# Kernel optimization log

Hardware: AMD Instinct MI355X
Metric: run time of the kernel (lower is better)

Reference implementation:

```python
import jax, jax.numpy as jnp
import numpy as np

B, T, D, H = 4, 2048, 1024, 16
HD = D // H  # head_dim = 64


def setup_inputs() -> dict:
    key = jax.random.key(0)
    ks = jax.random.split(key, 9)
    s = 1.0 / np.sqrt(D)
    return {
        "x": jax.random.normal(ks[0], (B, T, D), dtype=jnp.float32),
        "Wq": jax.random.normal(ks[1], (D, D), dtype=jnp.float32) * s,
        "bq": jax.random.normal(ks[2], (D,), dtype=jnp.float32) * 0.01,
        "Wk": jax.random.normal(ks[3], (D, D), dtype=jnp.float32) * s,
        "bk": jax.random.normal(ks[4], (D,), dtype=jnp.float32) * 0.01,
        "Wv": jax.random.normal(ks[5], (D, D), dtype=jnp.float32) * s,
        "bv": jax.random.normal(ks[6], (D,), dtype=jnp.float32) * 0.01,
        "Wp": jax.random.normal(ks[7], (D, D), dtype=jnp.float32) * s,
        "bp": jax.random.normal(ks[8], (D,), dtype=jnp.float32) * 0.01,
    }


def reference(x, Wq, bq, Wk, bk, Wv, bv, Wp, bp):
    # Linear projections (weights stored as [in, out]; torch Linear is x @ W.T + b,
    # here we store the already-transposed matrix so math is identical)
    q = (x @ Wq + bq).reshape(B, T, H, HD).transpose(0, 2, 1, 3)  # [B,H,T,HD]
    k = (x @ Wk + bk).reshape(B, T, H, HD).transpose(0, 2, 1, 3)
    v = (x @ Wv + bv).reshape(B, T, H, HD).transpose(0, 2, 1, 3)

    scores = jnp.einsum("bhqd,bhkd->bhqk", q, k) / jnp.sqrt(jnp.float32(HD))
    causal = jnp.tril(jnp.ones((T, T), dtype=bool))  # keep lower triangle
    scores = jnp.where(causal, scores, -jnp.inf)
    attn = jax.nn.softmax(scores, axis=-1)  # dropout is identity at eval
    out = jnp.einsum("bhqk,bhkd->bhqd", attn, v)  # [B,H,T,HD]
    out = out.transpose(0, 2, 1, 3).reshape(B, T, D)
    return out @ Wp + bp
```

## Files before the change

kernel.cpp:

```cpp
#include <hip/hip_runtime.h>
#include <hip/hip_bf16.h>

#define BB 4
#define TT 2048
#define DD 1024
#define HH 16
#define HD 64
#define MM (BB*TT)

typedef __attribute__((ext_vector_type(8))) _Float16 f16x8;
typedef __attribute__((ext_vector_type(4))) float f32x4;

static __device__ __forceinline__ void gload_lds16(const void* g, void* l) {
  __builtin_amdgcn_global_load_lds((const __attribute__((address_space(1))) void*)g,
                                   (__attribute__((address_space(3))) void*)l, 16, 0, 0);
}

__global__ __launch_bounds__(256) void cvt_f16(const float* __restrict__ in,
                                               _Float16* __restrict__ out, int n8) {
  int i = blockIdx.x * 256 + threadIdx.x;
  if (i >= n8) return;
  const f32x4* p = (const f32x4*)in;
  f32x4 a = p[2*i];
  f32x4 b = p[2*i+1];
  f16x8 r;
  r[0]=(_Float16)a[0]; r[1]=(_Float16)a[1]; r[2]=(_Float16)a[2]; r[3]=(_Float16)a[3];
  r[4]=(_Float16)b[0]; r[5]=(_Float16)b[1]; r[6]=(_Float16)b[2]; r[7]=(_Float16)b[3];
  *(f16x8*)(out + (size_t)8*i) = r;
}

__global__ __launch_bounds__(256) void transpose_cvt(
    const float* __restrict__ W0, const float* __restrict__ W1,
    const float* __restrict__ W2, const float* __restrict__ W3,
    _Float16* __restrict__ O0, _Float16* __restrict__ O1,
    _Float16* __restrict__ O2, _Float16* __restrict__ O3) {
  const float* W; _Float16* O;
  switch (blockIdx.z) {
    case 0: W = W0; O = O0; break;
    case 1: W = W1; O = O1; break;
    case 2: W = W2; O = O2; break;
    default: W = W3; O = O3; break;
  }
  __shared__ float tile[32][33];
  int bx = blockIdx.x * 32, by = blockIdx.y * 32;
  int tx = threadIdx.x, ty = threadIdx.y;
#pragma unroll
  for (int i = 0; i < 4; i++)
    tile[ty + 8*i][tx] = W[(size_t)(by + ty + 8*i) * DD + bx + tx];
  __syncthreads();
#pragma unroll
  for (int i = 0; i < 4; i++)
    O[(size_t)(bx + ty + 8*i) * DD + by + tx] = (_Float16)tile[tx][ty + 8*i];
}

template<bool OUT_F32>
static __device__ __forceinline__ void gemm_body(
    const _Float16* __restrict__ A, const _Float16* __restrict__ Bt,
    const float* __restrict__ bias, void* __restrict__ Cv) {
  const int K = 1024, N = 1024;
  __shared__ __align__(16) _Float16 Alds[128*32];
  __shared__ __align__(16) _Float16 Blds[128*32];
  int tid = threadIdx.x;
  int wid = tid >> 6, lane = tid & 63;
  int m0 = blockIdx.y * 128, n0 = blockIdx.x * 128;
  int wr = wid >> 1, wc = wid & 1;
  int lr = lane & 15, lk = lane >> 4;

  f32x4 zf = {0.f, 0.f, 0.f, 0.f};
  f32x4 acc[4][4];
#pragma unroll
  for (int m = 0; m < 4; m++)
#pragma unroll
    for (int n = 0; n < 4; n++) acc[m][n] = zf;

  int c0 = wid * 2;
  int srow = c0 * 16 + (lane >> 2);
  int skc  = (lane & 3) * 8;
  const _Float16* gA0 = A  + (size_t)(m0 + srow) * K + skc;
  const _Float16* gA1 = gA0 + 16 * K;
  const _Float16* gB0 = Bt + (size_t)(n0 + srow) * K + skc;
  const _Float16* gB1 = gB0 + 16 * K;
  _Float16* lA0 = Alds + c0 * 512;
  _Float16* lA1 = Alds + (c0 + 1) * 512;
  _Float16* lB0 = Blds + c0 * 512;
  _Float16* lB1 = Blds + (c0 + 1) * 512;

  for (int k0 = 0; k0 < K; k0 += 32) {
    __syncthreads();
    gload_lds16(gA0 + k0, lA0);
    gload_lds16(gA1 + k0, lA1);
    gload_lds16(gB0 + k0, lB0);
    gload_lds16(gB1 + k0, lB1);
    __syncthreads();
    f16x8 af[4], bf[4];
#pragma unroll
    for (int m = 0; m < 4; m++)
      af[m] = *(const f16x8*)&Alds[(wr*64 + m*16 + lr)*32 + lk*8];
#pragma unroll
    for (int n = 0; n < 4; n++)
      bf[n] = *(const f16x8*)&Blds[(wc*64 + n*16 + lr)*32 + lk*8];
#pragma unroll
    for (int m = 0; m < 4; m++)
#pragma unroll
      for (int n = 0; n < 4; n++)
        acc[m][n] = __builtin_amdgcn_mfma_f32_16x16x32_f16(af[m], bf[n], acc[m][n], 0, 0, 0);
  }

#pragma unroll
  for (int n = 0; n < 4; n++) {
    int col = n0 + wc*64 + n*16 + lr;
    float bs = bias[col];
#pragma unroll
    for (int m = 0; m < 4; m++) {
      int row = m0 + wr*64 + m*16 + lk*4;
#pragma unroll
      for (int r = 0; r < 4; r++) {
        float v = acc[m][n][r] + bs;
        if (OUT_F32) ((float*)Cv)[(size_t)(row + r) * N + col] = v;
        else         ((_Float16*)Cv)[(size_t)(row + r) * N + col] = (_Float16)v;
      }
    }
  }
}

__global__ __launch_bounds__(256) void gemm_qkv(
    const _Float16* __restrict__ X,
    const _Float16* __restrict__ WqT, const _Float16* __restrict__ WkT,
    const _Float16* __restrict__ WvT,
    const float* __restrict__ bq, const float* __restrict__ bk,
    const float* __restrict__ bv,
    _Float16* __restrict__ Qo, _Float16* __restrict__ Ko, _Float16* __restrict__ Vo) {
  const _Float16* Bt; const float* bias; _Float16* C;
  if (blockIdx.z == 0)      { Bt = WqT; bias = bq; C = Qo; }
  else if (blockIdx.z == 1) { Bt = WkT; bias = bk; C = Ko; }
  else                      { Bt = WvT; bias = bv; C = Vo; }
  gemm_body<false>(X, Bt, bias, C);
}

__global__ __launch_bounds__(256) void gemm_proj(
    const _Float16* __restrict__ Ain, const _Float16* __restrict__ WpT,
    const float* __restrict__ bp, float* __restrict__ out) {
  gemm_body<true>(Ain, WpT, bp, out);
}

__global__ __launch_bounds__(256, 2) void attn_fwd(
    const _Float16* __restrict__ Q, const _Float16* __restrict__ Kg,
    const _Float16* __restrict__ Vg, _Float16* __restrict__ O) {
  __shared__ __align__(16) _Float16 Klds[2*4096];
  __shared__ __align__(16) _Float16 Vt[2*4608];
  __shared__ __align__(16) _Float16 Plds[4*32*72];

  const int tid = threadIdx.x;
  const int wid = tid >> 6, lane = tid & 63;
  const int lr = lane & 15, lk = lane >> 4;
  const int bh = blockIdx.y, b = bh >> 4, h = bh & 15;
  const size_t base = (size_t)b * TT * DD + h * HD;
  const float sc = 0.18033688011112042f;

  const int krow  = 16*wid + (lane >> 3);
  const int kchnk = ((lane & 7) ^ (lane >> 3)) * 8;
  const int kg0 = krow*DD + kchnk, kg1 = (krow+8)*DD + kchnk;
  const int kl0 = 16*wid*64,       kl1 = (16*wid+8)*64;
  const int vch = lane & 7;
  const int vg0 = krow*DD + vch*8, vg1 = (krow+8)*DD + vch*8;

  _Float16* Pw = Plds + wid*32*72;

  for (int qs = 0; qs < 2; ++qs) {
    const int qt = qs ? (15 - (int)blockIdx.x) : (int)blockIdx.x;
    const int jmax = 2*qt + 1;

    f16x8 qf[2][2];
#pragma unroll
    for (int t = 0; t < 2; ++t) {
      const size_t qr = base + (size_t)(qt*128 + wid*32 + t*16 + lr) * DD;
#pragma unroll
      for (int hh2 = 0; hh2 < 2; ++hh2)
        qf[t][hh2] = *(const f16x8*)&Q[qr + hh2*32 + lk*8];
    }

    f32x4 zf = {0.f, 0.f, 0.f, 0.f};
    f32x4 o[2][4];
    float m[2][4], l[2][4];
#pragma unroll
    for (int t = 0; t < 2; ++t)
#pragma unroll
      for (int f = 0; f < 4; ++f) o[t][f] = zf;
#pragma unroll
    for (int t = 0; t < 2; ++t)
#pragma unroll
      for (int r = 0; r < 4; ++r) { m[t][r] = -1e30f; l[t][r] = 0.f; }

    {
      gload_lds16(Kg + base + kg0, Klds + kl0);
      gload_lds16(Kg + base + kg1, Klds + kl1);
      f16x8 v0 = *(const f16x8*)(Vg + base + vg0);
      f16x8 v1 = *(const f16x8*)(Vg + base + vg1);
#pragma unroll
      for (int u = 0; u < 8; ++u) {
        int d = vch*8 + u;
        int jx0 = (krow & 7)     | ((((krow>>3)     ^ (d>>3)) & 7) << 3);
        int jx1 = ((krow+8) & 7) | (((((krow+8)>>3) ^ (d>>3)) & 7) << 3);
        Vt[d*72 + jx0] = v0[u];
        Vt[d*72 + jx1] = v1[u];
      }
      __syncthreads();
    }

    int bsel = 0;
    for (int jt = 0; jt <= jmax; ++jt) {
      const bool pf = (jt < jmax);
      f16x8 vr0, vr1;
      if (pf) {
        const size_t nb = base + (size_t)(jt+1) * 64 * DD;
        _Float16* kd = Klds + (bsel^1)*4096;
        gload_lds16(Kg + nb + kg0, kd + kl0);
        gload_lds16(Kg + nb + kg1, kd + kl1);
        vr0 = *(const f16x8*)(Vg + nb + vg0);
        vr1 = *(const f16x8*)(Vg + nb + vg1);
      }

      const _Float16* Kb = Klds + bsel*4096;
      f32x4 s[2][4];
      __builtin_amdgcn_s_setprio(1);
#pragma unroll
      for (int f = 0; f < 4; ++f) {
        const int row = 16*f + lr;
        f16x8 kf0 = *(const f16x8*)&Kb[row*64 + ((lk    ) ^ (lr & 7))*8];
        f16x8 kf1 = *(const f16x8*)&Kb[row*64 + ((lk + 4) ^ (lr & 7))*8];
#pragma unroll
        for (int t = 0; t < 2; ++t) {
          f32x4 z = zf;
          z = __builtin_amdgcn_mfma_f32_16x16x32_f16(qf[t][0], kf0, z, 0, 0, 0);
          z = __builtin_amdgcn_mfma_f32_16x16x32_f16(qf[t][1], kf1, z, 0, 0, 0);
          s[t][f] = z;
        }
      }
      __builtin_amdgcn_s_setprio(0);

#pragma unroll
      for (int t = 0; t < 2; ++t) {
        const int qmin = qt*128 + wid*32 + t*16;
        if (64*jt + 64 > qmin) {
#pragma unroll
          for (int f = 0; f < 4; ++f)
#pragma unroll
            for (int r = 0; r < 4; ++r) {
              int jg = 64*jt + 16*f + lr;
              int qg = qmin + lk*4 + r;
              s[t][f][r] = (jg <= qg) ? s[t][f][r] * sc : -1e30f;
            }
        } else {
#pragma unroll
          for (int f = 0; f < 4; ++f)
#pragma unroll
            for (int r = 0; r < 4; ++r) s[t][f][r] *= sc;
        }
        float alpha[4];
#pragma unroll
        for (int r = 0; r < 4; ++r) {
          float v = fmaxf(fmaxf(s[t][0][r], s[t][1][r]), fmaxf(s[t][2][r], s[t][3][r]));
          v = fmaxf(v, __shfl_xor(v, 1));
          v = fmaxf(v, __shfl_xor(v, 2));
          v = fmaxf(v, __shfl_xor(v, 4));
          v = fmaxf(v, __shfl_xor(v, 8));
          float mn = fmaxf(m[t][r], v);
          alpha[r] = exp2f(m[t][r] - mn);
          m[t][r] = mn;
        }
#pragma unroll
        for (int r = 0; r < 4; ++r) {
          float sum = 0.f;
#pragma unroll
          for (int f = 0; f < 4; ++f) {
            float p = exp2f(s[t][f][r] - m[t][r]);
            s[t][f][r] = p;
            sum += p;
          }
          sum += __shfl_xor(sum, 1);
          sum += __shfl_xor(sum, 2);
          sum += __shfl_xor(sum, 4);
          sum += __shfl_xor(sum, 8);
          l[t][r] = l[t][r] * alpha[r] + sum;
#pragma unroll
          for (int f = 0; f < 4; ++f) o[t][f][r] *= alpha[r];
        }
#pragma unroll
        for (int f = 0; f < 4; ++f)
#pragma unroll
          for (int r = 0; r < 4; ++r)
            Pw[(t*16 + lk*4 + r)*72 + f*16 + lr] = (_Float16)s[t][f][r];
      }

      f16x8 pa[2][2];
#pragma unroll
      for (int t = 0; t < 2; ++t)
#pragma unroll
        for (int hh2 = 0; hh2 < 2; ++hh2)
          pa[t][hh2] = *(const f16x8*)&Pw[(t*16 + lr)*72 + hh2*32 + lk*8];

      const _Float16* Vb = Vt + bsel*4608;
      __builtin_amdgcn_s_setprio(1);
#pragma unroll
      for (int f = 0; f < 4; ++f) {
        int d0 = f*16 + lr;
        int cx = (d0 >> 3) & 7;
        f16x8 vf0 = *(const f16x8*)&Vb[d0*72 + (((0*4 + lk) ^ cx) << 3)];
        f16x8 vf1 = *(const f16x8*)&Vb[d0*72 + (((1*4 + lk) ^ cx) << 3)];
#pragma unroll
        for (int t = 0; t < 2; ++t) {
          o[t][f] = __builtin_amdgcn_mfma_f32_16x16x32_f16(pa[t][0], vf0, o[t][f], 0, 0, 0);
          o[t][f] = __builtin_amdgcn_mfma_f32_16x16x32_f16(pa[t][1], vf1, o[t][f], 0, 0, 0);
        }
      }
      __builtin_amdgcn_s_setprio(0);

      if (pf) {
        _Float16* vd = Vt + (bsel^1)*4608;
#pragma unroll
        for (int u = 0; u < 8; ++u) {
          int d = vch*8 + u;
          int jx0 = (krow & 7)     | ((((krow>>3)     ^ (d>>3)) & 7) << 3);
          int jx1 = ((krow+8) & 7) | (((((krow+8)>>3) ^ (d>>3)) & 7) << 3);
          vd[d*72 + jx0] = vr0[u];
          vd[d*72 + jx1] = vr1[u];
        }
      }
      __syncthreads();
      bsel ^= 1;
    }

#pragma unroll
    for (int t = 0; t < 2; ++t) {
      float inv[4];
#pragma unroll
      for (int r = 0; r < 4; ++r) inv[r] = 1.f / l[t][r];
#pragma unroll
      for (int f = 0; f < 4; ++f) {
        int d = 16*f + lr;
#pragma unroll
        for (int r = 0; r < 4; ++r) {
          int qg = qt*128 + wid*32 + t*16 + lk*4 + r;
          O[base + (size_t)qg * DD + d] = (_Float16)(o[t][f][r] * inv[r]);
        }
      }
    }
    __syncthreads();
  }
}

extern "C" void kernel_launch(void* const* d_in, const int* in_sizes, int n_in,
                              void* d_out, int out_size, void* d_ws, size_t ws_size,
                              hipStream_t stream) {
  const float* x  = (const float*)d_in[0];
  const float* Wq = (const float*)d_in[1];
  const float* bq = (const float*)d_in[2];
  const float* Wk = (const float*)d_in[3];
  const float* bk = (const float*)d_in[4];
  const float* Wv = (const float*)d_in[5];
  const float* bv = (const float*)d_in[6];
  const float* Wp = (const float*)d_in[7];
  const float* bp = (const float*)d_in[8];
  float* out = (float*)d_out;

  const size_t XN = (size_t)MM * DD;
  const size_t WN = (size_t)DD * DD;
  _Float16* ws  = (_Float16*)d_ws;
  _Float16* Xb  = ws;
  _Float16* WqT = ws + XN;
  _Float16* WkT = WqT + WN;
  _Float16* WvT = WkT + WN;
  _Float16* WpT = WvT + WN;
  _Float16* Qb  = WpT + WN;
  _Float16* Kb  = Qb + XN;
  _Float16* Vb  = Kb + XN;
  _Float16* Ab  = Xb;

  cvt_f16<<<dim3((unsigned)(XN/8/256)), 256, 0, stream>>>(x, Xb, (int)(XN/8));
  transpose_cvt<<<dim3(32, 32, 4), dim3(32, 8), 0, stream>>>(Wq, Wk, Wv, Wp,
                                                             WqT, WkT, WvT, WpT);
  gemm_qkv<<<dim3(8, 64, 3), 256, 0, stream>>>(Xb, WqT, WkT, WvT, bq, bk, bv,
                                               Qb, Kb, Vb);
  attn_fwd<<<dim3(8, 64), 256, 0, stream>>>(Qb, Kb, Vb, Ab);
  gemm_proj<<<dim3(8, 64), 256, 0, stream>>>(Ab, WpT, bp, out);
}
```

Baseline: 335.2 us.

## Emit transposed V and prescaled Q from QKV GEMM; simplify attention loads

The QKV GEMM epilogue now writes V transposed per (batch, head) and folds the softmax scale into Q. This lets the attention kernel load V with async global-to-LDS copies instead of a register transpose, and drop the per-score multiply. Attention also stops pairing light and heavy query tiles, launching one block per tile with a higher occupancy hint, and skips the online-softmax rescale unless the running max grows by more than a threshold. The cost is uneven causal work across blocks, strided 4-element stores in the V epilogue, and less exact max tracking, which is still correct but risks precision loss.

```diff
diff --git a/kernel.cpp b/kernel.cpp
--- a/kernel.cpp
+++ b/kernel.cpp
@@ -9,7 +9,10 @@
 #define MM (BB*TT)
 
 typedef __attribute__((ext_vector_type(8))) _Float16 f16x8;
+typedef __attribute__((ext_vector_type(4))) _Float16 f16x4;
 typedef __attribute__((ext_vector_type(4))) float f32x4;
+
+#define QSCALE 0.18033688011112042f
 
 static __device__ __forceinline__ void gload_lds16(const void* g, void* l) {
   __builtin_amdgcn_global_load_lds((const __attribute__((address_space(1))) void*)g,
@@ -53,10 +56,9 @@
     O[(size_t)(bx + ty + 8*i) * DD + by + tx] = (_Float16)tile[tx][ty + 8*i];
 }
 
-template<bool OUT_F32>
 static __device__ __forceinline__ void gemm_body(
     const _Float16* __restrict__ A, const _Float16* __restrict__ Bt,
-    const float* __restrict__ bias, void* __restrict__ Cv) {
+    const float* __restrict__ bias, void* __restrict__ Cv, int mode) {
   const int K = 1024, N = 1024;
   __shared__ __align__(16) _Float16 Alds[128*32];
   __shared__ __align__(16) _Float16 Blds[128*32];
@@ -112,12 +114,27 @@
     float bs = bias[col];
 #pragma unroll
     for (int m = 0; m < 4; m++) {
-      int row = m0 + wr*64 + m*16 + lk*4;
-#pragma unroll
-      for (int r = 0; r < 4; r++) {
-        float v = acc[m][n][r] + bs;
-        if (OUT_F32) ((float*)Cv)[(size_t)(row + r) * N + col] = v;
-        else         ((_Float16*)Cv)[(size_t)(row + r) * N + col] = (_Float16)v;
+      int rowg = m0 + wr*64 + m*16 + lk*4;
+      if (mode == 2) {
+        int b = rowg >> 11, t = rowg & 2047;
+        size_t idx = ((size_t)(b*1024 + col) << 11) + t;
+        f16x4 pk;
+#pragma unroll
+        for (int r = 0; r < 4; r++) pk[r] = (_Float16)(acc[m][n][r] + bs);
+        *(f16x4*)&((_Float16*)Cv)[idx] = pk;
+      } else if (mode == 3) {
+#pragma unroll
+        for (int r = 0; r < 4; r++)
+          ((float*)Cv)[(size_t)(rowg + r) * N + col] = acc[m][n][r] + bs;
+      } else if (mode == 1) {
+#pragma unroll
+        for (int r = 0; r < 4; r++)
+          ((_Float16*)Cv)[(size_t)(rowg + r) * N + col] =
+              (_Float16)((acc[m][n][r] + bs) * QSCALE);
+      } else {
+#pragma unroll
+        for (int r = 0; r < 4; r++)
+          ((_Float16*)Cv)[(size_t)(rowg + r) * N + col] = (_Float16)(acc[m][n][r] + bs);
       }
     }
   }
@@ -129,223 +146,208 @@
     const _Float16* __restrict__ WvT,
     const float* __restrict__ bq, const float* __restrict__ bk,
     const float* __restrict__ bv,
-    _Float16* __restrict__ Qo, _Float16* __restrict__ Ko, _Float16* __restrict__ Vo) {
-  const _Float16* Bt; const float* bias; _Float16* C;
-  if (blockIdx.z == 0)      { Bt = WqT; bias = bq; C = Qo; }
-  else if (blockIdx.z == 1) { Bt = WkT; bias = bk; C = Ko; }
-  else                      { Bt = WvT; bias = bv; C = Vo; }
-  gemm_body<false>(X, Bt, bias, C);
+    _Float16* __restrict__ Qo, _Float16* __restrict__ Ko, _Float16* __restrict__ Vto) {
+  const _Float16* Bt; const float* bias; _Float16* C; int mode;
+  if (blockIdx.z == 0)      { Bt = WqT; bias = bq; C = Qo;  mode = 1; }
+  else if (blockIdx.z == 1) { Bt = WkT; bias = bk; C = Ko;  mode = 0; }
+  else                      { Bt = WvT; bias = bv; C = Vto; mode = 2; }
+  gemm_body(X, Bt, bias, C, mode);
 }
 
 __global__ __launch_bounds__(256) void gemm_proj(
     const _Float16* __restrict__ Ain, const _Float16* __restrict__ WpT,
     const float* __restrict__ bp, float* __restrict__ out) {
-  gemm_body<true>(Ain, WpT, bp, out);
-}
-
-__global__ __launch_bounds__(256, 2) void attn_fwd(
+  gemm_body(Ain, WpT, bp, out, 3);
+}
+
+__global__ __launch_bounds__(256, 3) void attn_fwd(
     const _Float16* __restrict__ Q, const _Float16* __restrict__ Kg,
-    const _Float16* __restrict__ Vg, _Float16* __restrict__ O) {
+    const _Float16* __restrict__ Vt, _Float16* __restrict__ O) {
   __shared__ __align__(16) _Float16 Klds[2*4096];
-  __shared__ __align__(16) _Float16 Vt[2*4608];
+  __shared__ __align__(16) _Float16 Vlds[2*4096];
   __shared__ __align__(16) _Float16 Plds[4*32*72];
 
   const int tid = threadIdx.x;
   const int wid = tid >> 6, lane = tid & 63;
   const int lr = lane & 15, lk = lane >> 4;
   const int bh = blockIdx.y, b = bh >> 4, h = bh & 15;
-  const size_t base = (size_t)b * TT * DD + h * HD;
-  const float sc = 0.18033688011112042f;
+  const size_t base  = (size_t)b * TT * DD + h * HD;
+  const size_t vbase = (size_t)bh * HD * TT;
 
   const int krow  = 16*wid + (lane >> 3);
   const int kchnk = ((lane & 7) ^ (lane >> 3)) * 8;
-  const int kg0 = krow*DD + kchnk, kg1 = (krow+8)*DD + kchnk;
-  const int kl0 = 16*wid*64,       kl1 = (16*wid+8)*64;
-  const int vch = lane & 7;
-  const int vg0 = krow*DD + vch*8, vg1 = (krow+8)*DD + vch*8;
+  const int kg0 = krow*DD + kchnk, kg1 = kg0 + 8*DD;
+  const int vg0 = krow*TT + kchnk, vg1 = vg0 + 8*TT;
+  const int kl0 = 16*wid*64,       kl1 = kl0 + 8*64;
 
   _Float16* Pw = Plds + wid*32*72;
 
-  for (int qs = 0; qs < 2; ++qs) {
-    const int qt = qs ? (15 - (int)blockIdx.x) : (int)blockIdx.x;
-    const int jmax = 2*qt + 1;
-
-    f16x8 qf[2][2];
+  const int qt = blockIdx.x;
+  const int jmax = 2*qt + 1;
+
+  f16x8 qf[2][2];
+#pragma unroll
+  for (int t = 0; t < 2; ++t) {
+    const size_t qr = base + (size_t)(qt*128 + wid*32 + t*16 + lr) * DD;
+#pragma unroll
+    for (int hh2 = 0; hh2 < 2; ++hh2)
+      qf[t][hh2] = *(const f16x8*)&Q[qr + hh2*32 + lk*8];
+  }
+
+  f32x4 zf = {0.f, 0.f, 0.f, 0.f};
+  f32x4 o[2][4];
+  float m[2][4], l[2][4];
+#pragma unroll
+  for (int t = 0; t < 2; ++t)
+#pragma unroll
+    for (int f = 0; f < 4; ++f) o[t][f] = zf;
+#pragma unroll
+  for (int t = 0; t < 2; ++t)
+#pragma unroll
+    for (int r = 0; r < 4; ++r) { m[t][r] = -1e30f; l[t][r] = 0.f; }
+
+  gload_lds16(Kg + base + kg0, Klds + kl0);
+  gload_lds16(Kg + base + kg1, Klds + kl1);
+  gload_lds16(Vt + vbase + vg0, Vlds + kl0);
+  gload_lds16(Vt + vbase + vg1, Vlds + kl1);
+  __syncthreads();
+
+  int bsel = 0;
+  for (int jt = 0; jt <= jmax; ++jt) {
+    if (jt < jmax) {
+      const size_t kb = base + (size_t)(jt+1) * 64 * DD;
+      const size_t vb = vbase + (size_t)(jt+1) * 64;
+      _Float16* kd = Klds + (bsel^1)*4096;
+      _Float16* vd = Vlds + (bsel^1)*4096;
+      gload_lds16(Kg + kb + kg0, kd + kl0);
+      gload_lds16(Kg + kb + kg1, kd + kl1);
+      gload_lds16(Vt + vb + vg0, vd + kl0);
+      gload_lds16(Vt + vb + vg1, vd + kl1);
+    }
+
+    const _Float16* Kb = Klds + bsel*4096;
+    f32x4 s[2][4];
+    __builtin_amdgcn_s_setprio(1);
+#pragma unroll
+    for (int f = 0; f < 4; ++f) {
+      const int row = 16*f + lr;
+      f16x8 kf0 = *(const f16x8*)&Kb[row*64 + ((lk    ) ^ (lr & 7))*8];
+      f16x8 kf1 = *(const f16x8*)&Kb[row*64 + ((lk + 4) ^ (lr & 7))*8];
+#pragma unroll
+      for (int t = 0; t < 2; ++t) {
+        f32x4 z = zf;
+        z = __builtin_amdgcn_mfma_f32_16x16x32_f16(qf[t][0], kf0, z, 0, 0, 0);
+        z = __builtin_amdgcn_mfma_f32_16x16x32_f16(qf[t][1], kf1, z, 0, 0, 0);
+        s[t][f] = z;
+      }
+    }
+    __builtin_amdgcn_s_setprio(0);
+
 #pragma unroll
     for (int t = 0; t < 2; ++t) {
-      const size_t qr = base + (size_t)(qt*128 + wid*32 + t*16 + lr) * DD;
-#pragma unroll
-      for (int hh2 = 0; hh2 < 2; ++hh2)
-        qf[t][hh2] = *(const f16x8*)&Q[qr + hh2*32 + lk*8];
-    }
-
-    f32x4 zf = {0.f, 0.f, 0.f, 0.f};
-    f32x4 o[2][4];
-    float m[2][4], l[2][4];
+      const int qmin = qt*128 + wid*32 + t*16;
+      if (64*jt + 64 > qmin) {
+#pragma unroll
+        for (int f = 0; f < 4; ++f)
+#pragma unroll
+          for (int r = 0; r < 4; ++r) {
+            int jg = 64*jt + 16*f + lr;
+            int qg = qmin + lk*4 + r;
+            if (jg > qg) s[t][f][r] = -1e30f;
+          }
+      }
+    }
+
+    float vmax[2][4];
+    bool grow = false;
 #pragma unroll
     for (int t = 0; t < 2; ++t)
 #pragma unroll
-      for (int f = 0; f < 4; ++f) o[t][f] = zf;
-#pragma unroll
-    for (int t = 0; t < 2; ++t)
-#pragma unroll
-      for (int r = 0; r < 4; ++r) { m[t][r] = -1e30f; l[t][r] = 0.f; }
-
-    {
-      gload_lds16(Kg + base + kg0, Klds + kl0);
-      gload_lds16(Kg + base + kg1, Klds + kl1);
-      f16x8 v0 = *(const f16x8*)(Vg + base + vg0);
-      f16x8 v1 = *(const f16x8*)(Vg + base + vg1);
-#pragma unroll
-      for (int u = 0; u < 8; ++u) {
-        int d = vch*8 + u;
-        int jx0 = (krow & 7)     | ((((krow>>3)     ^ (d>>3)) & 7) << 3);
-        int jx1 = ((krow+8) & 7) | (((((krow+8)>>3) ^ (d>>3)) & 7) << 3);
-        Vt[d*72 + jx0] = v0[u];
-        Vt[d*72 + jx1] = v1[u];
-      }
-      __syncthreads();
-    }
-
-    int bsel = 0;
-    for (int jt = 0; jt <= jmax; ++jt) {
-      const bool pf = (jt < jmax);
-      f16x8 vr0, vr1;
-      if (pf) {
-        const size_t nb = base + (size_t)(jt+1) * 64 * DD;
-        _Float16* kd = Klds + (bsel^1)*4096;
-        gload_lds16(Kg + nb + kg0, kd + kl0);
-        gload_lds16(Kg + nb + kg1, kd + kl1);
-        vr0 = *(const f16x8*)(Vg + nb + vg0);
-        vr1 = *(const f16x8*)(Vg + nb + vg1);
-      }
-
-      const _Float16* Kb = Klds + bsel*4096;
-      f32x4 s[2][4];
-      __builtin_amdgcn_s_setprio(1);
-#pragma unroll
-      for (int f = 0; f < 4; ++f) {
-        const int row = 16*f + lr;
-        f16x8 kf0 = *(const f16x8*)&Kb[row*64 + ((lk    ) ^ (lr & 7))*8];
-        f16x8 kf1 = *(const f16x8*)&Kb[row*64 + ((lk + 4) ^ (lr & 7))*8];
-#pragma unroll
-        for (int t = 0; t < 2; ++t) {
-          f32x4 z = zf;
-          z = __builtin_amdgcn_mfma_f32_16x16x32_f16(qf[t][0], kf0, z, 0, 0, 0);
-          z = __builtin_amdgcn_mfma_f32_16x16x32_f16(qf[t][1], kf1, z, 0, 0, 0);
-          s[t][f] = z;
-        }
-      }
-      __builtin_amdgcn_s_setprio(0);
-
-#pragma unroll
-      for (int t = 0; t < 2; ++t) {
-        const int qmin = qt*128 + wid*32 + t*16;
-        if (64*jt + 64 > qmin) {
-#pragma unroll
-          for (int f = 0; f < 4; ++f)
-#pragma unroll
-            for (int r = 0; r < 4; ++r) {
-              int jg = 64*jt + 16*f + lr;
-              int qg = qmin + lk*4 + r;
-              s[t][f][r] = (jg <= qg) ? s[t][f][r] * sc : -1e30f;
-            }
-        } else {
-#pragma unroll
-          for (int f = 0; f < 4; ++f)
-#pragma unroll
-            for (int r = 0; r < 4; ++r) s[t][f][r] *= sc;
-        }
-        float alpha[4];
-#pragma unroll
-        for (int r = 0; r < 4; ++r) {
-          float v = fmaxf(fmaxf(s[t][0][r], s[t][1][r]), fmaxf(s[t][2][r], s[t][3][r]));
-          v = fmaxf(v, __shfl_xor(v, 1));
-          v = fmaxf(v, __shfl_xor(v, 2));
-          v = fmaxf(v, __shfl_xor(v, 4));
-          v = fmaxf(v, __shfl_xor(v, 8));
-          float mn = fmaxf(m[t][r], v);
-          alpha[r] = exp2f(m[t][r] - mn);
+      for (int r = 0; r < 4; ++r) {
+        float v = fmaxf(fmaxf(s[t][0][r], s[t][1][r]), fmaxf(s[t][2][r], s[t][3][r]));
+        v = fmaxf(v, __shfl_xor(v, 1));
+        v = fmaxf(v, __shfl_xor(v, 2));
+        v = fmaxf(v, __shfl_xor(v, 4));
+        v = fmaxf(v, __shfl_xor(v, 8));
+        vmax[t][r] = v;
+        grow = grow || (v > m[t][r] + 8.f);
+      }
+    const bool anygrow = (__ballot(grow) != 0ull);
+
+#pragma unroll
+    for (int t = 0; t < 2; ++t) {
+#pragma unroll
+      for (int r = 0; r < 4; ++r) {
+        float alpha = 1.f;
+        if (anygrow) {
+          float mn = fmaxf(m[t][r], vmax[t][r]);
+          alpha = exp2f(m[t][r] - mn);
           m[t][r] = mn;
         }
-#pragma unroll
-        for (int r = 0; r < 4; ++r) {
-          float sum = 0.f;
-#pragma unroll
-          for (int f = 0; f < 4; ++f) {
-            float p = exp2f(s[t][f][r] - m[t][r]);
-            s[t][f][r] = p;
-            sum += p;
-          }
-          sum += __shfl_xor(sum, 1);
-          sum += __shfl_xor(sum, 2);
-          sum += __shfl_xor(sum, 4);
-          sum += __shfl_xor(sum, 8);
-          l[t][r] = l[t][r] * alpha[r] + sum;
-#pragma unroll
-          for (int f = 0; f < 4; ++f) o[t][f][r] *= alpha[r];
+        float sum = 0.f;
+#pragma unroll
+        for (int f = 0; f < 4; ++f) {
+          float p = exp2f(s[t][f][r] - m[t][r]);
+          s[t][f][r] = p;
+          sum += p;
         }
-#pragma unroll
-        for (int f = 0; f < 4; ++f)
-#pragma unroll
-          for (int r = 0; r < 4; ++r)
-            Pw[(t*16 + lk*4 + r)*72 + f*16 + lr] = (_Float16)s[t][f][r];
-      }
-
-      f16x8 pa[2][2];
-#pragma unroll
-      for (int t = 0; t < 2; ++t)
-#pragma unroll
-        for (int hh2 = 0; hh2 < 2; ++hh2)
-          pa[t][hh2] = *(const f16x8*)&Pw[(t*16 + lr)*72 + hh2*32 + lk*8];
-
-      const _Float16* Vb = Vt + bsel*4608;
-      __builtin_amdgcn_s_setprio(1);
-#pragma unroll
-      for (int f = 0; f < 4; ++f) {
-        int d0 = f*16 + lr;
-        int cx = (d0 >> 3) & 7;
-        f16x8 vf0 = *(const f16x8*)&Vb[d0*72 + (((0*4 + lk) ^ cx) << 3)];
-        f16x8 vf1 = *(const f16x8*)&Vb[d0*72 + (((1*4 + lk) ^ cx) << 3)];
-#pragma unroll
-        for (int t = 0; t < 2; ++t) {
-          o[t][f] = __builtin_amdgcn_mfma_f32_16x16x32_f16(pa[t][0], vf0, o[t][f], 0, 0, 0);
-          o[t][f] = __builtin_amdgcn_mfma_f32_16x16x32_f16(pa[t][1], vf1, o[t][f], 0, 0, 0);
+        sum += __shfl_xor(sum, 1);
+        sum += __shfl_xor(sum, 2);
+        sum += __shfl_xor(sum, 4);
+        sum += __shfl_xor(sum, 8);
+        l[t][r] = l[t][r] * alpha + sum;
+        if (anygrow) {
+#pragma unroll
+          for (int f = 0; f < 4; ++f) o[t][f][r] *= alpha;
         }
       }
-      __builtin_amdgcn_s_setprio(0);
-
-      if (pf) {
-        _Float16* vd = Vt + (bsel^1)*4608;
-#pragma unroll
-        for (int u = 0; u < 8; ++u) {
-          int d = vch*8 + u;
-          int jx0 = (krow & 7)     | ((((krow>>3)     ^ (d>>3)) & 7) << 3);
-          int jx1 = ((krow+8) & 7) | (((((krow+8)>>3) ^ (d>>3)) & 7) << 3);
-          vd[d*72 + jx0] = vr0[u];
-          vd[d*72 + jx1] = vr1[u];
-        }
-      }
-      __syncthreads();
-      bsel ^= 1;
-    }
-
-#pragma unroll
-    for (int t = 0; t < 2; ++t) {
-      float inv[4];
-#pragma unroll
-      for (int r = 0; r < 4; ++r) inv[r] = 1.f / l[t][r];
-#pragma unroll
-      for (int f = 0; f < 4; ++f) {
-        int d = 16*f + lr;
-#pragma unroll
-        for (int r = 0; r < 4; ++r) {
-          int qg = qt*128 + wid*32 + t*16 + lk*4 + r;
-          O[base + (size_t)qg * DD + d] = (_Float16)(o[t][f][r] * inv[r]);
-        }
-      }
-    }
+#pragma unroll
+      for (int f = 0; f < 4; ++f)
+#pragma unroll
+        for (int r = 0; r < 4; ++r)
+          Pw[(t*16 + lk*4 + r)*72 + f*16 + lr] = (_Float16)s[t][f][r];
+    }
+
+    f16x8 pa[2][2];
+#pragma unroll
+    for (int t = 0; t < 2; ++t)
+#pragma unroll
+      for (int hh2 = 0; hh2 < 2; ++hh2)
+        pa[t][hh2] = *(const f16x8*)&Pw[(t*16 + lr)*72 + hh2*32 + lk*8];
+
+    const _Float16* Vb = Vlds + bsel*4096;
+    __builtin_amdgcn_s_setprio(1);
+#pragma unroll
+    for (int f = 0; f < 4; ++f) {
+      const int row = 16*f + lr;
+      f16x8 vf0 = *(const f16x8*)&Vb[row*64 + ((lk    ) ^ (lr & 7))*8];
+      f16x8 vf1 = *(const f16x8*)&Vb[row*64 + ((lk + 4) ^ (lr & 7))*8];
+#pragma unroll
+      for (int t = 0; t < 2; ++t) {
+        o[t][f] = __builtin_amdgcn_mfma_f32_16x16x32_f16(pa[t][0], vf0, o[t][f], 0, 0, 0);
+        o[t][f] = __builtin_amdgcn_mfma_f32_16x16x32_f16(pa[t][1], vf1, o[t][f], 0, 0, 0);
+      }
+    }
+    __builtin_amdgcn_s_setprio(0);
+
     __syncthreads();
+    bsel ^= 1;
+  }
+
+#pragma unroll
+  for (int t = 0; t < 2; ++t) {
+    float inv[4];
+#pragma unroll
+    for (int r = 0; r < 4; ++r) inv[r] = 1.f / l[t][r];
+#pragma unroll
+    for (int f = 0; f < 4; ++f) {
+      int d = 16*f + lr;
+#pragma unroll
+      for (int r = 0; r < 4; ++r) {
+        int qg = qt*128 + wid*32 + t*16 + lk*4 + r;
+        O[base + (size_t)qg * DD + d] = (_Float16)(o[t][f][r] * inv[r]);
+      }
+    }
   }
 }
 
@@ -373,14 +375,14 @@
   _Float16* WpT = WvT + WN;
   _Float16* Qb  = WpT + WN;
   _Float16* Kb  = Qb + XN;
-  _Float16* Vb  = Kb + XN;
+  _Float16* Vbt = Kb + XN;
   _Float16* Ab  = Xb;
 
   cvt_f16<<<dim3((unsigned)(XN/8/256)), 256, 0, stream>>>(x, Xb, (int)(XN/8));
   transpose_cvt<<<dim3(32, 32, 4), dim3(32, 8), 0, stream>>>(Wq, Wk, Wv, Wp,
                                                              WqT, WkT, WvT, WpT);
   gemm_qkv<<<dim3(8, 64, 3), 256, 0, stream>>>(Xb, WqT, WkT, WvT, bq, bk, bv,
-                                               Qb, Kb, Vb);
-  attn_fwd<<<dim3(8, 64), 256, 0, stream>>>(Qb, Kb, Vb, Ab);
+                                               Qb, Kb, Vbt);
+  attn_fwd<<<dim3(16, 64), 256, 0, stream>>>(Qb, Kb, Vbt, Ab);
   gemm_proj<<<dim3(8, 64), 256, 0, stream>>>(Ab, WpT, bp, out);
 }
```

Result: slower. 453.1 us (+35.2%).
